# Optimization experiments

Measured on AMD Instinct MI355X. Metric: run time of the kernel, lower is better.

Reference implementation:

```python
import jax, jax.numpy as jnp
import numpy as np


def _diag_gather(x):
    # out[b,c,h,w] = x[b,c,h,(h+w)%W]; then transpose last two dims and flatten
    B, C, H, W = x.shape
    idx = (jnp.arange(H)[:, None] + jnp.arange(W)[None, :]) % W
    g = jnp.take_along_axis(x, idx[None, None], axis=3)  # [B,C,H,W]
    return g.transpose(0, 1, 3, 2).reshape(B, C, H * W)


def _antidiag_gather(x):
    B, C, H, W = x.shape
    idx = (jnp.arange(W)[None, :] - jnp.arange(H)[:, None]) % W
    g = jnp.take_along_axis(x, idx[None, None], axis=3)
    return g.transpose(0, 1, 3, 2).reshape(B, C, H * W)


def _diag_scatter(flat, shape):
    # exact inverse of _diag_gather (per-row circular-shift permutation)
    B, C, H, W = shape
    t = flat.reshape(B, C, W, H).transpose(0, 1, 3, 2)  # [B,C,H,W]
    inv = (jnp.arange(W)[None, :] - jnp.arange(H)[:, None]) % W
    return jnp.take_along_axis(t, inv[None, None], axis=3)


def _antidiag_scatter(flat, shape):
    B, C, H, W = shape
    t = flat.reshape(B, C, W, H).transpose(0, 1, 3, 2)
    inv = (jnp.arange(W)[None, :] + jnp.arange(H)[:, None]) % W
    return jnp.take_along_axis(t, inv[None, None], axis=3)


def cross_scan(x):
    # x: [B,C,H,W] -> xs: [B,8,C,L]; 8 scan directions (row, col, flips, diag, antidiag, flips)
    B, C, H, W = x.shape
    L = H * W
    xf = x.reshape(B, C, L)
    xt = x.transpose(0, 1, 3, 2).reshape(B, C, L)
    xd = _diag_gather(x)
    xa = _antidiag_gather(x)
    return jnp.stack(
        [xf, xt, xf[..., ::-1], xt[..., ::-1], xd, xa, xd[..., ::-1], xa[..., ::-1]],
        axis=1,
    )


def cross_merge(ys):
    # ys: [B,8,D,H,W] -> y: [B,D,L]
    B, K, D, H, W = ys.shape
    L = H * W
    ys = ys.reshape(B, K, D, L)
    a = ys[:, 0:2] + ys[:, 2:4][..., ::-1]
    y = a[:, 0] + a[:, 1].reshape(B, D, W, H).transpose(0, 1, 3, 2).reshape(B, D, L)
    b = ys[:, 4:6] + ys[:, 6:8][..., ::-1]
    y = y + _diag_scatter(b[:, 0], (B, D, H, W)).reshape(B, D, L)
    y = y + _antidiag_scatter(b[:, 1], (B, D, H, W)).reshape(B, D, L)
    return y


def selective_scan(u, delta, A, Bs, Cs, Ds):
    # u, delta: [B,KD,L]; A: [KD,N]; Bs, Cs: [B,K,N,L]; Ds: [KD]
    Bn, KD, L = u.shape
    K = Bs.shape[1]
    Dd = KD // K
    N = A.shape[1]
    dA = jnp.exp(delta[:, :, None, :] * A[None, :, :, None])  # [B,KD,N,L]
    Bexp = jnp.broadcast_to(Bs[:, :, None], (Bn, K, Dd, N, L)).reshape(Bn, KD, N, L)
    Cexp = jnp.broadcast_to(Cs[:, :, None], (Bn, K, Dd, N, L)).reshape(Bn, KD, N, L)
    dBu = delta[:, :, None, :] * Bexp * u[:, :, None, :]

    def comb(c1, c2):
        a1, b1 = c1
        a2, b2 = c2
        return a2 * a1, a2 * b1 + b2

    _, h = jax.lax.associative_scan(comb, (dA, dBu), axis=-1)  # h: [B,KD,N,L]
    return jnp.sum(Cexp * h, axis=2) + Ds[None, :, None] * u


def setup_inputs() -> dict:
    key = jax.random.key(0)
    ks = jax.random.split(key, 8)
    B, D, H, W = 1, 96, 64, 64
    K, N, R = 8, 16, 6
    return {
        "x": jax.random.normal(ks[0], (B, D, H, W), jnp.float32),
        "x_proj_weight": jax.random.normal(ks[1], (K, R + 2 * N, D), jnp.float32) * 0.05,
        "dt_projs_weight": jax.random.normal(ks[2], (K, D, R), jnp.float32) * 0.1,
        "dt_projs_bias": jax.random.normal(ks[3], (K, D), jnp.float32) * 0.1,
        "A_logs": jax.random.uniform(ks[4], (K * D, N), jnp.float32),
        "Ds": jax.random.normal(ks[5], (K * D,), jnp.float32),
        "out_norm_weight": jnp.ones((D,), jnp.float32),
        "out_norm_bias": jnp.zeros((D,), jnp.float32),
    }


def reference(x, x_proj_weight, dt_projs_weight, dt_projs_bias, A_logs, Ds,
              out_norm_weight, out_norm_bias):
    B, D, H, W = x.shape
    K, _, R = dt_projs_weight.shape
    N = A_logs.shape[1]
    L = H * W

    xs = cross_scan(x)  # [B,K,D,L]
    x_dbl = jnp.einsum("bkdl,kcd->bkcl", xs, x_proj_weight)  # [B,K,R+2N,L]
    dts, Bs, Cs = jnp.split(x_dbl, [R, R + N], axis=2)
    dts = jnp.einsum("bkrl,kdr->bkdl", dts, dt_projs_weight)  # [B,K,D,L]

    u = xs.reshape(B, K * D, L)
    delta = jax.nn.softplus(dts.reshape(B, K * D, L)
                            + dt_projs_bias.reshape(-1)[None, :, None])
    A = -jnp.exp(A_logs)  # [KD,N]

    ys = selective_scan(u, delta, A, Bs, Cs, Ds)  # [B,KD,L]
    y = cross_merge(ys.reshape(B, K, D, H, W))  # [B,D,L]

    # out_norm (v0): LayerNorm over channel dim
    y = y.transpose(0, 2, 1)  # [B,L,D]
    mu = jnp.mean(y, axis=-1, keepdims=True)
    var = jnp.var(y, axis=-1, keepdims=True)
    y = (y - mu) * jax.lax.rsqrt(var + 1e-5) * out_norm_weight + out_norm_bias
    return y.reshape(B, H, W, D)
```

## Files before the change

### kernel.cpp

```cpp
#include <hip/hip_runtime.h>
#include <math.h>

#define D_ 96
#define L_ 4096
#define K_ 8
#define N_ 16
#define R_ 6
#define CDBL 38
#define DL_ (D_ * L_)

#define REPN(M) M(0) M(1) M(2) M(3) M(4) M(5) M(6) M(7) \
                M(8) M(9) M(10) M(11) M(12) M(13) M(14) M(15)

__device__ __forceinline__ float softplusf(float x) {
    return (x > 20.f) ? x : log1pf(__expf(x));
}

__device__ __forceinline__ int src_index(int k, int l) {
    int h = l & 63, w = l >> 6;
    int lp = 4095 - l;
    int hp = lp & 63, wp = lp >> 6;
    switch (k) {
    case 0: return l;
    case 1: return (h << 6) + w;
    case 2: return lp;
    case 3: return (hp << 6) + wp;
    case 4: return (h << 6) + ((h + w) & 63);
    case 5: return (h << 6) + ((w - h) & 63);
    case 6: return (hp << 6) + ((hp + wp) & 63);
    default: return (hp << 6) + ((wp - hp) & 63);
    }
}

__global__ __launch_bounds__(256) void k_xdbl(const float* __restrict__ x,
                                              const float* __restrict__ wproj,
                                              float* __restrict__ xdbl) {
    __shared__ float tile[64][100];
    __shared__ float wlds[40 * D_];
    int bid = blockIdx.x;
    int swz = (bid & 7) * 64 + (bid >> 3);
    int k = swz >> 6;
    int l0 = (swz & 63) * 64;

    for (int e = threadIdx.x; e < 40 * D_; e += 256)
        wlds[e] = (e < CDBL * D_) ? wproj[k * CDBL * D_ + e] : 0.f;
    for (int e = threadIdx.x; e < D_ * 64; e += 256) {
        int d = e >> 6, li = e & 63;
        tile[li][d] = x[d * L_ + src_index(k, l0 + li)];
    }
    __syncthreads();

    int lt = threadIdx.x & 63;
    int cg = threadIdx.x >> 6;
    float acc[10];
    #pragma unroll
    for (int j = 0; j < 10; ++j) acc[j] = 0.f;
    for (int d4 = 0; d4 < D_; d4 += 4) {
        float4 tv = *(const float4*)&tile[lt][d4];
        #pragma unroll
        for (int j = 0; j < 10; ++j) {
            int c = cg + 4 * j;
            float4 wv = *(const float4*)&wlds[c * D_ + d4];
            acc[j] = fmaf(tv.x, wv.x, acc[j]);
            acc[j] = fmaf(tv.y, wv.y, acc[j]);
            acc[j] = fmaf(tv.z, wv.z, acc[j]);
            acc[j] = fmaf(tv.w, wv.w, acc[j]);
        }
    }
    #pragma unroll
    for (int j = 0; j < 10; ++j) {
        int c = cg + 4 * j;
        if (c < CDBL) xdbl[(k * CDBL + c) * L_ + l0 + lt] = acc[j];
    }
}


#if __has_builtin(__builtin_amdgcn_update_dpp)
#define HAVE_DPP 1
template<int CTRL, int RM>
__device__ __forceinline__ float updpp(float oldv, float src) {
    int r = __builtin_amdgcn_update_dpp(__builtin_bit_cast(int, oldv),
                                        __builtin_bit_cast(int, src),
                                        CTRL, RM, 0xF, false);
    return __builtin_bit_cast(float, r);
}
#else
#define HAVE_DPP 0
#endif

__global__ __launch_bounds__(256, 3) void k_scan(const float* __restrict__ xdbl,
                                                 const float* __restrict__ dtw,
                                                 const float* __restrict__ dtb,
                                                 const float* __restrict__ alogs,
                                                 const float* __restrict__ dsv_,
                                                 const float* __restrict__ x,
                                                 float* __restrict__ ys) {
    int bid = blockIdx.x;
    int k = bid & 7;
    int d = bid >> 3;
    int kd = k * D_ + d;
    int t = threadIdx.x;
    int lane = t & 63, wv = t >> 6;
    int l0t = t * 16;

    __shared__ float An_s[16];
    __shared__ float agg_a[4][16], agg_b[4][16];
    if (t < 16) An_s[t] = -expf(alogs[kd * N_ + t]);

#define DECL(n) float sA##n, sB##n;
    REPN(DECL)
#undef DECL
#define DECL(n) float d##n, u##n, y##n;
    REPN(DECL)
#undef DECL

    const float* xr = xdbl + k * CDBL * L_;
    const float2* wp2 = (const float2*)(dtw + kd * R_);
    const float2 w01 = wp2[0], w23 = wp2[1], w45 = wp2[2];
    const float bias = dtb[kd];
#define DLTQ(j, i0, i1, i2, i3) { \
    const float4 r0 = *(const float4*)(xr + 0 * L_ + l0t + j * 4); \
    const float4 r1 = *(const float4*)(xr + 1 * L_ + l0t + j * 4); \
    const float4 r2 = *(const float4*)(xr + 2 * L_ + l0t + j * 4); \
    const float4 r3 = *(const float4*)(xr + 3 * L_ + l0t + j * 4); \
    const float4 r4 = *(const float4*)(xr + 4 * L_ + l0t + j * 4); \
    const float4 r5 = *(const float4*)(xr + 5 * L_ + l0t + j * 4); \
    float s; \
    s = fmaf(w01.x, r0.x, bias); s = fmaf(w01.y, r1.x, s); s = fmaf(w23.x, r2.x, s); \
    s = fmaf(w23.y, r3.x, s); s = fmaf(w45.x, r4.x, s); s = fmaf(w45.y, r5.x, s); \
    d##i0 = softplusf(s); \
    s = fmaf(w01.x, r0.y, bias); s = fmaf(w01.y, r1.y, s); s = fmaf(w23.x, r2.y, s); \
    s = fmaf(w23.y, r3.y, s); s = fmaf(w45.x, r4.y, s); s = fmaf(w45.y, r5.y, s); \
    d##i1 = softplusf(s); \
    s = fmaf(w01.x, r0.z, bias); s = fmaf(w01.y, r1.z, s); s = fmaf(w23.x, r2.z, s); \
    s = fmaf(w23.y, r3.z, s); s = fmaf(w45.x, r4.z, s); s = fmaf(w45.y, r5.z, s); \
    d##i2 = softplusf(s); \
    s = fmaf(w01.x, r0.w, bias); s = fmaf(w01.y, r1.w, s); s = fmaf(w23.x, r2.w, s); \
    s = fmaf(w23.y, r3.w, s); s = fmaf(w45.x, r4.w, s); s = fmaf(w45.y, r5.w, s); \
    d##i3 = softplusf(s); }
    DLTQ(0, 0, 1, 2, 3)
    DLTQ(1, 4, 5, 6, 7)
    DLTQ(2, 8, 9, 10, 11)
    DLTQ(3, 12, 13, 14, 15)
#undef DLTQ

    const float* xd = x + d * L_;
#define UG(i) u##i = xd[src_index(k, l0t + i)]; y##i = 0.f;
    REPN(UG)
#undef UG

    __syncthreads();

    const float* Bptr = xdbl + (k * CDBL + R_) * L_ + l0t;
    const float* Cptr = Bptr + N_ * L_;

#define PHA_E(i, Bc) { float a = __expf(d##i * An); \
    float b = d##i * (Bc) * u##i; \
    rb = fmaf(a, rb, b); ra *= a; }
#define PHA(n) { \
    const float An = An_s[n]; \
    const float* Bn = Bptr + n * L_; \
    const float4 b0 = *(const float4*)(Bn + 0), b1 = *(const float4*)(Bn + 4); \
    const float4 b2 = *(const float4*)(Bn + 8), b3 = *(const float4*)(Bn + 12); \
    float ra = 1.f, rb = 0.f; \
    PHA_E(0, b0.x) PHA_E(1, b0.y) PHA_E(2, b0.z) PHA_E(3, b0.w) \
    PHA_E(4, b1.x) PHA_E(5, b1.y) PHA_E(6, b1.z) PHA_E(7, b1.w) \
    PHA_E(8, b2.x) PHA_E(9, b2.y) PHA_E(10, b2.z) PHA_E(11, b2.w) \
    PHA_E(12, b3.x) PHA_E(13, b3.y) PHA_E(14, b3.z) PHA_E(15, b3.w) \
    sA##n = ra; sB##n = rb; \
    asm volatile("" ::: "memory"); }
    REPN(PHA)
#undef PHA
#undef PHA_E

#if HAVE_DPP
#define SSTN(n) { float pa = updpp<SC_CTRL, SC_RM>(1.f, sA##n); \
                  float pb = updpp<SC_CTRL, SC_RM>(0.f, sB##n); \
                  sB##n = fmaf(sA##n, pb, sB##n); sA##n *= pa; }
#define SC_CTRL 0x111
#define SC_RM 0xF
    REPN(SSTN)
#undef SC_CTRL
#undef SC_RM
#define SC_CTRL 0x112
#define SC_RM 0xF
    REPN(SSTN)
#undef SC_CTRL
#undef SC_RM
#define SC_CTRL 0x114
#define SC_RM 0xF
    REPN(SSTN)
#undef SC_CTRL
#undef SC_RM
#define SC_CTRL 0x118
#define SC_RM 0xF
    REPN(SSTN)
#undef SC_CTRL
#undef SC_RM
#define SC_CTRL 0x142
#define SC_RM 0xA
    REPN(SSTN)
#undef SC_CTRL
#undef SC_RM
#define SC_CTRL 0x143
#define SC_RM 0xC
    REPN(SSTN)
#undef SC_CTRL
#undef SC_RM
#undef SSTN
#else
#define PBF(n) { float pa = __shfl_up(sA##n, off); float pb = __shfl_up(sB##n, off); \
    if (lane >= off) { sB##n = fmaf(sA##n, pb, sB##n); sA##n *= pa; } }
    for (int off = 1; off < 64; off <<= 1) { REPN(PBF) }
#undef PBF
#endif

#define PPREF(n) { float ia = sA##n, ib = sB##n; \
    float ea = __shfl_up(ia, 1); float eb = __shfl_up(ib, 1); \
    if (lane == 0) { ea = 1.f; eb = 0.f; } \
    if (lane == 63) { agg_a[wv][n] = ia; agg_b[wv][n] = ib; } \
    sA##n = ea; sB##n = eb; }
    REPN(PPREF)
#undef PPREF
    __syncthreads();

#define PC(n) { float cb = 0.f; \
    for (int w2 = 0; w2 < wv; ++w2) cb = fmaf(agg_a[w2][n], cb, agg_b[w2][n]); \
    sA##n = fmaf(sA##n, cb, sB##n); }
    REPN(PC)
#undef PC

#define PHD_E(i, Bc, Cc) { float a = __expf(d##i * An); \
    float b = d##i * (Bc) * u##i; \
    h = fmaf(a, h, b); y##i = fmaf((Cc), h, y##i); }
#define PHD(n) { \
    const float An = An_s[n]; float h = sA##n; \
    const float* Bn = Bptr + n * L_; const float* Cn = Cptr + n * L_; \
    const float4 b0 = *(const float4*)(Bn + 0), b1 = *(const float4*)(Bn + 4); \
    const float4 b2 = *(const float4*)(Bn + 8), b3 = *(const float4*)(Bn + 12); \
    const float4 c0 = *(const float4*)(Cn + 0), c1 = *(const float4*)(Cn + 4); \
    const float4 c2 = *(const float4*)(Cn + 8), c3 = *(const float4*)(Cn + 12); \
    PHD_E(0, b0.x, c0.x) PHD_E(1, b0.y, c0.y) PHD_E(2, b0.z, c0.z) PHD_E(3, b0.w, c0.w) \
    PHD_E(4, b1.x, c1.x) PHD_E(5, b1.y, c1.y) PHD_E(6, b1.z, c1.z) PHD_E(7, b1.w, c1.w) \
    PHD_E(8, b2.x, c2.x) PHD_E(9, b2.y, c2.y) PHD_E(10, b2.z, c2.z) PHD_E(11, b2.w, c2.w) \
    PHD_E(12, b3.x, c3.x) PHD_E(13, b3.y, c3.y) PHD_E(14, b3.z, c3.z) PHD_E(15, b3.w, c3.w) \
    asm volatile("" ::: "memory"); }
    REPN(PHD)
#undef PHD
#undef PHD_E

    const float dval = dsv_[kd];
#define YD(i) y##i = fmaf(dval, u##i, y##i);
    REPN(YD)
#undef YD
    float* yp = ys + kd * L_ + l0t;
    {
        float4 o;
        o.x = y0;  o.y = y1;  o.z = y2;  o.w = y3;  *(float4*)(yp + 0)  = o;
        o.x = y4;  o.y = y5;  o.z = y6;  o.w = y7;  *(float4*)(yp + 4)  = o;
        o.x = y8;  o.y = y9;  o.z = y10; o.w = y11; *(float4*)(yp + 8)  = o;
        o.x = y12; o.y = y13; o.z = y14; o.w = y15; *(float4*)(yp + 12) = o;
    }
}

__global__ __launch_bounds__(256) void k_merge_ln(const float* __restrict__ ys,
                                                  const float* __restrict__ gamma,
                                                  const float* __restrict__ beta,
                                                  float* __restrict__ out) {
    __shared__ float sm[32][D_ + 1];
    __shared__ float mu_s[32], rs_s[32];
    int l0 = blockIdx.x * 32;
    for (int e = threadIdx.x; e < 32 * D_; e += 256) {
        int li = e & 31, d = e >> 5;
        int l = l0 + li;
        int h = l >> 6, w = l & 63;
        int i1 = (w << 6) + h;
        int i4 = (((w - h) & 63) << 6) + h;
        int i5 = (((w + h) & 63) << 6) + h;
        const float* bd = ys + d * L_;
        float v = bd[0 * DL_ + l] + bd[2 * DL_ + 4095 - l]
                + bd[1 * DL_ + i1] + bd[3 * DL_ + 4095 - i1]
                + bd[4 * DL_ + i4] + bd[6 * DL_ + 4095 - i4]
                + bd[5 * DL_ + i5] + bd[7 * DL_ + 4095 - i5];
        sm[li][d] = v;
    }
    __syncthreads();
    int li2 = threadIdx.x >> 3, sub = threadIdx.x & 7;
    float s = 0.f, sq = 0.f;
    for (int d = sub; d < D_; d += 8) {
        float v = sm[li2][d];
        s += v; sq = fmaf(v, v, sq);
    }
    s += __shfl_xor(s, 1); sq += __shfl_xor(sq, 1);
    s += __shfl_xor(s, 2); sq += __shfl_xor(sq, 2);
    s += __shfl_xor(s, 4); sq += __shfl_xor(sq, 4);
    if (sub == 0) {
        float mu = s * (1.f / 96.f);
        float var = sq * (1.f / 96.f) - mu * mu;
        mu_s[li2] = mu;
        rs_s[li2] = rsqrtf(var + 1e-5f);
    }
    __syncthreads();
    for (int e = threadIdx.x; e < 32 * D_; e += 256) {
        int li = e / D_, d = e - li * D_;
        float v = (sm[li][d] - mu_s[li]) * rs_s[li];
        out[(l0 + li) * D_ + d] = fmaf(v, gamma[d], beta[d]);
    }
}

extern "C" void kernel_launch(void* const* d_in, const int* in_sizes, int n_in,
                              void* d_out, int out_size, void* d_ws, size_t ws_size,
                              hipStream_t stream) {
    const float* x     = (const float*)d_in[0];
    const float* wproj = (const float*)d_in[1];
    const float* dtw   = (const float*)d_in[2];
    const float* dtb   = (const float*)d_in[3];
    const float* alogs = (const float*)d_in[4];
    const float* dsv   = (const float*)d_in[5];
    const float* gamma = (const float*)d_in[6];
    const float* beta  = (const float*)d_in[7];
    float* out = (float*)d_out;
    float* ws  = (float*)d_ws;

    float* xdbl = ws;
    float* ysb  = ws + 1245184;

    hipLaunchKernelGGL(k_xdbl, dim3(512), dim3(256), 0, stream, x, wproj, xdbl);
    hipLaunchKernelGGL(k_scan, dim3(768), dim3(256), 0, stream,
                       xdbl, dtw, dtb, alogs, dsv, x, ysb);
    hipLaunchKernelGGL(k_merge_ln, dim3(128), dim3(256), 0, stream,
                       ysb, gamma, beta, out);
}
```

Measured before the change: 108.3 us.

## Split scan across 512 threads with 8 steps each, use exp2 and prescaled inputs

The scan kernel now uses 512 threads per block, each covering 8 sequence positions instead of 16. This halves per-thread register state and adds parallelism, in exchange for a larger cross-wave prefix combine over 8 waves. The exponent is computed with a native exp2 on A prescaled by log2(e). delta*u is folded into u once, and the D skip term initialises y. The projection kernel drops the LDS staging of weights and reads them directly from global memory with a wave-uniform channel group, removing a shared-memory fill but relying on cache for weight reuse.

```diff
diff --git a/kernel.cpp b/kernel.cpp
--- a/kernel.cpp
+++ b/kernel.cpp
@@ -11,6 +11,13 @@
 
 #define REPN(M) M(0) M(1) M(2) M(3) M(4) M(5) M(6) M(7) \
                 M(8) M(9) M(10) M(11) M(12) M(13) M(14) M(15)
+#define REP8(M) M(0) M(1) M(2) M(3) M(4) M(5) M(6) M(7)
+
+#if __has_builtin(__builtin_amdgcn_exp2f)
+#define EXP2(x) __builtin_amdgcn_exp2f(x)
+#else
+#define EXP2(x) exp2f(x)
+#endif
 
 __device__ __forceinline__ float softplusf(float x) {
     return (x > 20.f) ? x : log1pf(__expf(x));
@@ -36,14 +43,11 @@
                                               const float* __restrict__ wproj,
                                               float* __restrict__ xdbl) {
     __shared__ float tile[64][100];
-    __shared__ float wlds[40 * D_];
     int bid = blockIdx.x;
     int swz = (bid & 7) * 64 + (bid >> 3);
     int k = swz >> 6;
     int l0 = (swz & 63) * 64;
 
-    for (int e = threadIdx.x; e < 40 * D_; e += 256)
-        wlds[e] = (e < CDBL * D_) ? wproj[k * CDBL * D_ + e] : 0.f;
     for (int e = threadIdx.x; e < D_ * 64; e += 256) {
         int d = e >> 6, li = e & 63;
         tile[li][d] = x[d * L_ + src_index(k, l0 + li)];
@@ -51,7 +55,8 @@
     __syncthreads();
 
     int lt = threadIdx.x & 63;
-    int cg = threadIdx.x >> 6;
+    int cg = __builtin_amdgcn_readfirstlane(threadIdx.x >> 6);
+    const float* wk = wproj + k * CDBL * D_;
     float acc[10];
     #pragma unroll
     for (int j = 0; j < 10; ++j) acc[j] = 0.f;
@@ -60,11 +65,13 @@
         #pragma unroll
         for (int j = 0; j < 10; ++j) {
             int c = cg + 4 * j;
-            float4 wv = *(const float4*)&wlds[c * D_ + d4];
-            acc[j] = fmaf(tv.x, wv.x, acc[j]);
-            acc[j] = fmaf(tv.y, wv.y, acc[j]);
-            acc[j] = fmaf(tv.z, wv.z, acc[j]);
-            acc[j] = fmaf(tv.w, wv.w, acc[j]);
+            if (c < CDBL) {
+                float4 wv = *(const float4*)&wk[c * D_ + d4];
+                acc[j] = fmaf(tv.x, wv.x, acc[j]);
+                acc[j] = fmaf(tv.y, wv.y, acc[j]);
+                acc[j] = fmaf(tv.z, wv.z, acc[j]);
+                acc[j] = fmaf(tv.w, wv.w, acc[j]);
+            }
         }
     }
     #pragma unroll
@@ -88,7 +95,7 @@
 #define HAVE_DPP 0
 #endif
 
-__global__ __launch_bounds__(256, 3) void k_scan(const float* __restrict__ xdbl,
+__global__ __launch_bounds__(512, 6) void k_scan(const float* __restrict__ xdbl,
                                                  const float* __restrict__ dtw,
                                                  const float* __restrict__ dtb,
                                                  const float* __restrict__ alogs,
@@ -101,23 +108,25 @@
     int kd = k * D_ + d;
     int t = threadIdx.x;
     int lane = t & 63, wv = t >> 6;
-    int l0t = t * 16;
-
-    __shared__ float An_s[16];
-    __shared__ float agg_a[4][16], agg_b[4][16];
-    if (t < 16) An_s[t] = -expf(alogs[kd * N_ + t]);
+    int l0t = t * 8;
+
+    __shared__ float An2_s[16];
+    __shared__ float agg_a[8][16], agg_b[8][16];
+    if (t < 16)
+        An2_s[t] = -expf(alogs[kd * N_ + t]) * 1.44269504088896340736f;
 
 #define DECL(n) float sA##n, sB##n;
     REPN(DECL)
 #undef DECL
-#define DECL(n) float d##n, u##n, y##n;
-    REPN(DECL)
+#define DECL(i) float d##i, u##i, y##i;
+    REP8(DECL)
 #undef DECL
 
     const float* xr = xdbl + k * CDBL * L_;
     const float2* wp2 = (const float2*)(dtw + kd * R_);
     const float2 w01 = wp2[0], w23 = wp2[1], w45 = wp2[2];
     const float bias = dtb[kd];
+    const float dval = dsv_[kd];
 #define DLTQ(j, i0, i1, i2, i3) { \
     const float4 r0 = *(const float4*)(xr + 0 * L_ + l0t + j * 4); \
     const float4 r1 = *(const float4*)(xr + 1 * L_ + l0t + j * 4); \
@@ -140,13 +149,11 @@
     d##i3 = softplusf(s); }
     DLTQ(0, 0, 1, 2, 3)
     DLTQ(1, 4, 5, 6, 7)
-    DLTQ(2, 8, 9, 10, 11)
-    DLTQ(3, 12, 13, 14, 15)
 #undef DLTQ
 
     const float* xd = x + d * L_;
-#define UG(i) u##i = xd[src_index(k, l0t + i)]; y##i = 0.f;
-    REPN(UG)
+#define UG(i) u##i = xd[src_index(k, l0t + i)]; y##i = dval * u##i; u##i *= d##i;
+    REP8(UG)
 #undef UG
 
     __syncthreads();
@@ -154,19 +161,15 @@
     const float* Bptr = xdbl + (k * CDBL + R_) * L_ + l0t;
     const float* Cptr = Bptr + N_ * L_;
 
-#define PHA_E(i, Bc) { float a = __expf(d##i * An); \
-    float b = d##i * (Bc) * u##i; \
-    rb = fmaf(a, rb, b); ra *= a; }
+#define PHA_E(i, Bc) { float e = EXP2(d##i * An2); \
+    rb = fmaf(e, rb, u##i * (Bc)); ra *= e; }
 #define PHA(n) { \
-    const float An = An_s[n]; \
+    const float An2 = An2_s[n]; \
     const float* Bn = Bptr + n * L_; \
-    const float4 b0 = *(const float4*)(Bn + 0), b1 = *(const float4*)(Bn + 4); \
-    const float4 b2 = *(const float4*)(Bn + 8), b3 = *(const float4*)(Bn + 12); \
+    const float4 b0 = *(const float4*)(Bn), b1 = *(const float4*)(Bn + 4); \
     float ra = 1.f, rb = 0.f; \
     PHA_E(0, b0.x) PHA_E(1, b0.y) PHA_E(2, b0.z) PHA_E(3, b0.w) \
     PHA_E(4, b1.x) PHA_E(5, b1.y) PHA_E(6, b1.z) PHA_E(7, b1.w) \
-    PHA_E(8, b2.x) PHA_E(9, b2.y) PHA_E(10, b2.z) PHA_E(11, b2.w) \
-    PHA_E(12, b3.x) PHA_E(13, b3.y) PHA_E(14, b3.z) PHA_E(15, b3.w) \
     sA##n = ra; sB##n = rb; \
     asm volatile("" ::: "memory"); }
     REPN(PHA)
@@ -230,36 +233,25 @@
     REPN(PC)
 #undef PC
 
-#define PHD_E(i, Bc, Cc) { float a = __expf(d##i * An); \
-    float b = d##i * (Bc) * u##i; \
-    h = fmaf(a, h, b); y##i = fmaf((Cc), h, y##i); }
+#define PHD_E(i, Bc, Cc) { float e = EXP2(d##i * An2); \
+    h = fmaf(e, h, u##i * (Bc)); y##i = fmaf((Cc), h, y##i); }
 #define PHD(n) { \
-    const float An = An_s[n]; float h = sA##n; \
+    const float An2 = An2_s[n]; float h = sA##n; \
     const float* Bn = Bptr + n * L_; const float* Cn = Cptr + n * L_; \
-    const float4 b0 = *(const float4*)(Bn + 0), b1 = *(const float4*)(Bn + 4); \
-    const float4 b2 = *(const float4*)(Bn + 8), b3 = *(const float4*)(Bn + 12); \
-    const float4 c0 = *(const float4*)(Cn + 0), c1 = *(const float4*)(Cn + 4); \
-    const float4 c2 = *(const float4*)(Cn + 8), c3 = *(const float4*)(Cn + 12); \
+    const float4 b0 = *(const float4*)(Bn), b1 = *(const float4*)(Bn + 4); \
+    const float4 c0 = *(const float4*)(Cn), c1 = *(const float4*)(Cn + 4); \
     PHD_E(0, b0.x, c0.x) PHD_E(1, b0.y, c0.y) PHD_E(2, b0.z, c0.z) PHD_E(3, b0.w, c0.w) \
     PHD_E(4, b1.x, c1.x) PHD_E(5, b1.y, c1.y) PHD_E(6, b1.z, c1.z) PHD_E(7, b1.w, c1.w) \
-    PHD_E(8, b2.x, c2.x) PHD_E(9, b2.y, c2.y) PHD_E(10, b2.z, c2.z) PHD_E(11, b2.w, c2.w) \
-    PHD_E(12, b3.x, c3.x) PHD_E(13, b3.y, c3.y) PHD_E(14, b3.z, c3.z) PHD_E(15, b3.w, c3.w) \
     asm volatile("" ::: "memory"); }
     REPN(PHD)
 #undef PHD
 #undef PHD_E
 
-    const float dval = dsv_[kd];
-#define YD(i) y##i = fmaf(dval, u##i, y##i);
-    REPN(YD)
-#undef YD
     float* yp = ys + kd * L_ + l0t;
     {
         float4 o;
-        o.x = y0;  o.y = y1;  o.z = y2;  o.w = y3;  *(float4*)(yp + 0)  = o;
-        o.x = y4;  o.y = y5;  o.z = y6;  o.w = y7;  *(float4*)(yp + 4)  = o;
-        o.x = y8;  o.y = y9;  o.z = y10; o.w = y11; *(float4*)(yp + 8)  = o;
-        o.x = y12; o.y = y13; o.z = y14; o.w = y15; *(float4*)(yp + 12) = o;
+        o.x = y0; o.y = y1; o.z = y2; o.w = y3; *(float4*)(yp + 0) = o;
+        o.x = y4; o.y = y5; o.z = y6; o.w = y7; *(float4*)(yp + 4) = o;
     }
 }
 
@@ -326,7 +318,7 @@
     float* ysb  = ws + 1245184;
 
     hipLaunchKernelGGL(k_xdbl, dim3(512), dim3(256), 0, stream, x, wproj, xdbl);
-    hipLaunchKernelGGL(k_scan, dim3(768), dim3(256), 0, stream,
+    hipLaunchKernelGGL(k_scan, dim3(768), dim3(512), 0, stream,
                        xdbl, dtw, dtb, alogs, dsv, x, ysb);
     hipLaunchKernelGGL(k_merge_ln, dim3(128), dim3(256), 0, stream,
                        ysb, gamma, beta, out);
```

Result: slower. 116.2 us (+7.3%).
